# Kernel optimization log

Measured on AMD Instinct MI355X. Metric: run time of the kernel, lower is better.

Reference implementation:

```python
import jax, jax.numpy as jnp
import numpy as np
import math

B, S, D, H, DH = 2, 4096, 1024, 16, 64
CHUNK, RNDS, NBUCK, MLP = 128, 2, 64, 4096


def setup_inputs() -> dict:
    key = jax.random.key(0)
    ks = jax.random.split(key, 8)
    return {
        "inputs": jax.random.normal(ks[0], (B, S, D), jnp.float32),
        "ln1_scale": jnp.ones((D,), jnp.float32),
        "ln1_bias": jnp.zeros((D,), jnp.float32),
        "w_qk": jax.random.normal(ks[1], (D, H, DH), jnp.float32) * 0.02,
        "w_v": jax.random.normal(ks[2], (D, H, DH), jnp.float32) * 0.02,
        "w_out": jax.random.normal(ks[3], (H, DH, D), jnp.float32) * 0.02,
        "rotations": jax.random.normal(ks[4], (DH, RNDS, NBUCK // 2), jnp.float32),
        "ln2_scale": jnp.ones((D,), jnp.float32),
        "ln2_bias": jnp.zeros((D,), jnp.float32),
        "w_mlp1": jax.random.normal(ks[5], (D, MLP), jnp.float32) * 0.02,
        "b_mlp1": jnp.zeros((MLP,), jnp.float32),
        "w_mlp2": jax.random.normal(ks[6], (MLP, D), jnp.float32) * 0.02,
        "b_mlp2": jnp.zeros((D,), jnp.float32),
    }


def _layer_norm(x, scale, bias):
    mu = x.mean(-1, keepdims=True)
    var = ((x - mu) ** 2).mean(-1, keepdims=True)
    return (x - mu) / jnp.sqrt(var + 1e-6) * scale + bias


def _attend_one(q, k, v, buckets):
    # q,k,v: [S,DH]; buckets: [S] int. Sort by bucket (stable via position tiebreak),
    # chunk, attend to own chunk + 1 before + 1 after (look_both_side).
    nC = S // CHUNK
    order = jnp.argsort(buckets * S + jnp.arange(S))  # [S]
    undo = jnp.argsort(order)
    sq = q[order].reshape(nC, CHUNK, DH)
    sk = k[order].reshape(nC, CHUNK, DH)
    sv = v[order].reshape(nC, CHUNK, DH)
    st = order.reshape(nC, CHUNK)  # original token positions
    look = lambda x: jnp.concatenate([x, jnp.roll(x, 1, axis=0), jnp.roll(x, -1, axis=0)], axis=1)
    bk, bv = look(sk), look(sv)
    bt = look(st[..., None])[..., 0]
    dots = jnp.einsum('nqd,nkd->nqk', sq, bk) / math.sqrt(DH)
    # self_mask: a token attends to itself only if nothing else is available
    dots = dots - 1e5 * (st[:, :, None] == bt[:, None, :]).astype(dots.dtype)
    slog = jax.nn.logsumexp(dots, axis=-1)           # [nC,CHUNK]
    o = jnp.einsum('nqk,nkd->nqd', jax.nn.softmax(dots, axis=-1), bv)
    return o.reshape(S, DH)[undo], slog.reshape(S)[undo]


def _lsh_attention(qk, v, rotations):
    # qk,v: [B,H,S,DH]; shared-QK Reformer attention; keys are length-normalized.
    xn = qk / (jnp.linalg.norm(qk, axis=-1, keepdims=True) + 1e-6)
    rot = jnp.einsum('bhsd,drm->bhrsm', xn, rotations)          # [B,H,R,S,NBUCK/2]
    buckets = jnp.argmax(jnp.concatenate([rot, -rot], -1), -1)  # [B,H,R,S]
    rep = lambda x: jnp.broadcast_to(x[:, :, None], (B, H, RNDS, S, DH)).reshape(-1, S, DH)
    o, slog = jax.vmap(_attend_one)(rep(qk), rep(xn), rep(v), buckets.reshape(-1, S))
    o = o.reshape(B, H, RNDS, S, DH)
    slog = slog.reshape(B, H, RNDS, S)
    w = jax.nn.softmax(slog, axis=2)  # combine hash rounds by their logsumexp weight
    return (o * w[..., None]).sum(axis=2)  # [B,H,S,DH]


def reference(inputs, ln1_scale, ln1_bias, w_qk, w_v, w_out, rotations,
              ln2_scale, ln2_bias, w_mlp1, b_mlp1, w_mlp2, b_mlp2):
    x = _layer_norm(inputs, ln1_scale, ln1_bias)
    qk = jnp.einsum('bsd,dhe->bhse', x, w_qk)
    v = jnp.einsum('bsd,dhe->bhse', x, w_v)
    att = _lsh_attention(qk, v, rotations)
    x2 = inputs + jnp.einsum('bhse,hed->bsd', att, w_out)
    y = _layer_norm(x2, ln2_scale, ln2_bias)
    y = jax.nn.gelu(y @ w_mlp1 + b_mlp1) @ w_mlp2 + b_mlp2
    return x2 + y
```

## Files before the change

### kernel.cpp

```cpp
#include <hip/hip_runtime.h>
#include <hip/hip_bf16.h>


typedef short short8 __attribute__((ext_vector_type(8)));
typedef float f32x4 __attribute__((ext_vector_type(4)));
typedef unsigned short us4 __attribute__((ext_vector_type(4)));

__device__ __forceinline__ unsigned short f2bf(float f) {
  unsigned u = __builtin_bit_cast(unsigned, f);
  u += 0x7FFFu + ((u >> 16) & 1u);
  return (unsigned short)(u >> 16);
}

__device__ __forceinline__ float bf2f(unsigned short u) {
  return __builtin_bit_cast(float, ((unsigned)u) << 16);
}

__device__ __forceinline__ float gelu_f(float x) {
  float x3 = x * x * x;
  float t = tanhf(0.7978845608028654f * (x + 0.044715f * x3));
  return 0.5f * x * (1.0f + t);
}

__device__ __forceinline__ void load_lds16(const void* g, void* l) {
  __builtin_amdgcn_global_load_lds(
      (const __attribute__((address_space(1))) unsigned int*)g,
      (__attribute__((address_space(3))) unsigned int*)l, 16, 0, 0);
}

__global__ __launch_bounds__(256) void transpose_cast(
    const float* __restrict__ in, unsigned short* __restrict__ out, int R,
    int C) {
  __shared__ float tile[32][33];
  int ctiles = C >> 5;
  int bx = blockIdx.x % ctiles;
  int by = blockIdx.x / ctiles;
  int tx = threadIdx.x & 31;
  int ty = threadIdx.x >> 5;
#pragma unroll
  for (int i = 0; i < 32; i += 8)
    tile[ty + i][tx] = in[(size_t)(by * 32 + ty + i) * C + bx * 32 + tx];
  __syncthreads();
#pragma unroll
  for (int i = 0; i < 32; i += 8)
    out[(size_t)(bx * 32 + ty + i) * R + by * 32 + tx] = f2bf(tile[tx][ty + i]);
}

__global__ __launch_bounds__(256) void ln_bf16(const float* __restrict__ x,
                                               const float* __restrict__ sc,
                                               const float* __restrict__ bi,
                                               unsigned short* __restrict__ y) {
  int row = blockIdx.x, tid = threadIdx.x, lane = tid & 63, wv = tid >> 6;
  const float* xr = x + (size_t)row * 1024;
  float4 v = *(const float4*)(xr + tid * 4);
  float s1 = v.x + v.y + v.z + v.w;
  float s2 = v.x * v.x + v.y * v.y + v.z * v.z + v.w * v.w;
#pragma unroll
  for (int o = 1; o < 64; o <<= 1) {
    s1 += __shfl_xor(s1, o);
    s2 += __shfl_xor(s2, o);
  }
  __shared__ float a1[4], a2[4];
  if (lane == 0) {
    a1[wv] = s1;
    a2[wv] = s2;
  }
  __syncthreads();
  s1 = a1[0] + a1[1] + a1[2] + a1[3];
  s2 = a2[0] + a2[1] + a2[2] + a2[3];
  float mu = s1 * (1.f / 1024.f);
  float var = s2 * (1.f / 1024.f) - mu * mu;
  float rs = rsqrtf(var + 1e-6f);
  int c = tid * 4;
  us4 o4;
  o4.x = f2bf((v.x - mu) * rs * sc[c + 0] + bi[c + 0]);
  o4.y = f2bf((v.y - mu) * rs * sc[c + 1] + bi[c + 1]);
  o4.z = f2bf((v.z - mu) * rs * sc[c + 2] + bi[c + 2]);
  o4.w = f2bf((v.w - mu) * rs * sc[c + 3] + bi[c + 3]);
  *(us4*)(y + (size_t)row * 1024 + c) = o4;
}

#define GBM 128
#define GBN 128
#define GBK 32

template <int EPI>
__global__ __launch_bounds__(256) void gemm_bt(
    const unsigned short* __restrict__ A, const unsigned short* __restrict__ Bt,
    const float* __restrict__ bias, const float* __restrict__ res,
    float* __restrict__ Cf, unsigned short* __restrict__ Cb, int M, int N,
    int K) {
  __shared__ unsigned short sA[2][GBM * GBK];
  __shared__ unsigned short sB[2][GBN * GBK];
  const int nbx = N / GBN;
  const int nwg = gridDim.x;
  const int cpx = nwg >> 3;
  const int bid = blockIdx.x;
  const int swz = (bid & 7) * cpx + (bid >> 3);
  const int bx = swz % nbx;
  const int by = swz / nbx;
  const int tid = threadIdx.x;
  const int lane = tid & 63;
  const int wave = tid >> 6;
  const int wr = wave >> 1, wc = wave & 1;
  const unsigned short* Abase = A + (size_t)(by * GBM) * K;
  const unsigned short* Bbase = Bt + (size_t)(bx * GBN) * K;

  const int strow = wave * 32 + (lane >> 2);
  const int stcol = (lane & 3) * 8;
  const unsigned short* Ag = Abase + (size_t)strow * K + stcol;
  const unsigned short* Bg = Bbase + (size_t)strow * K + stcol;
  const int ldsoff = wave * 32 * GBK;
  const int ldsoff2 = ldsoff + 16 * GBK;

  f32x4 acc[4][4];
#pragma unroll
  for (int m = 0; m < 4; ++m)
#pragma unroll
    for (int n = 0; n < 4; ++n) {
      f32x4 z = {0.f, 0.f, 0.f, 0.f};
      acc[m][n] = z;
    }

  const int KT = K / GBK;
  load_lds16(Ag, &sA[0][ldsoff]);
  load_lds16(Ag + (size_t)16 * K, &sA[0][ldsoff2]);
  load_lds16(Bg, &sB[0][ldsoff]);
  load_lds16(Bg + (size_t)16 * K, &sB[0][ldsoff2]);
  __syncthreads();

  int cur = 0;
  const int arow = wr * 64 + (lane & 15);
  const int brow = wc * 64 + (lane & 15);
  const int koff = (lane >> 4) * 8;

  for (int kt = 0; kt < KT; ++kt) {
    if (kt + 1 < KT) {
      const unsigned short* An = Ag + (size_t)(kt + 1) * GBK;
      const unsigned short* Bn = Bg + (size_t)(kt + 1) * GBK;
      load_lds16(An, &sA[cur ^ 1][ldsoff]);
      load_lds16(An + (size_t)16 * K, &sA[cur ^ 1][ldsoff2]);
      load_lds16(Bn, &sB[cur ^ 1][ldsoff]);
      load_lds16(Bn + (size_t)16 * K, &sB[cur ^ 1][ldsoff2]);
    }
    short8 af[4], bfv[4];
#pragma unroll
    for (int m = 0; m < 4; ++m)
      af[m] = *(const short8*)&sA[cur][(arow + m * 16) * GBK + koff];
#pragma unroll
    for (int n = 0; n < 4; ++n)
      bfv[n] = *(const short8*)&sB[cur][(brow + n * 16) * GBK + koff];
#pragma unroll
    for (int m = 0; m < 4; ++m)
#pragma unroll
      for (int n = 0; n < 4; ++n)
        acc[m][n] = __builtin_amdgcn_mfma_f32_16x16x32_bf16(af[m], bfv[n],
                                                            acc[m][n], 0, 0, 0);
    __syncthreads();
    cur ^= 1;
  }

  const int r0 = by * GBM + wr * 64;
  const int c0 = bx * GBN + wc * 64;
#pragma unroll
  for (int m = 0; m < 4; ++m) {
#pragma unroll
    for (int n = 0; n < 4; ++n) {
#pragma unroll
      for (int i = 0; i < 4; ++i) {
        int rr = r0 + m * 16 + ((lane >> 4) << 2) + i;
        int cc = c0 + n * 16 + (lane & 15);
        float vacc = acc[m][n][i];
        if (EPI == 1) {
          float t = vacc + bias[cc];
          Cb[(size_t)rr * N + cc] = f2bf(gelu_f(t));
        } else if (EPI == 2) {
          float t = vacc + res[(size_t)rr * N + cc];
          if (bias != nullptr) t += bias[cc];
          Cf[(size_t)rr * N + cc] = t;
        } else if (EPI == 3) {
          Cf[(size_t)rr * N + cc] = vacc;
          Cb[(size_t)rr * N + cc] = f2bf(vacc);
        } else if (EPI == 4) {
          Cb[(size_t)rr * N + cc] = f2bf(vacc);
        }
      }
    }
  }
}

__global__ __launch_bounds__(256) void bucket_kernel(
    const float* __restrict__ qk, const float* __restrict__ rot,
    unsigned short* __restrict__ knb, int* __restrict__ buckets) {
  __shared__ float rotl[64 * 64];
  __shared__ float xnl[4][64];
  int tid = threadIdx.x, lane = tid & 63, wv = tid >> 6;
  for (int i = tid; i < 4096; i += 256) rotl[i] = rot[i];
  __syncthreads();
  for (int it = 0; it < 8; ++it) {
    int g = (it * 4096 + blockIdx.x) * 4 + wv;
    int bh = g >> 12;
    int s = g & 4095;
    int b = bh >> 4, h = bh & 15;
    size_t rowoff = (size_t)(b * 4096 + s) * 1024 + h * 64;
    float x = qk[rowoff + lane];
    float ss = x * x;
#pragma unroll
    for (int o = 1; o < 64; o <<= 1) ss += __shfl_xor(ss, o);
    float rn = 1.f / (sqrtf(ss) + 1e-6f);
    float xn = x * rn;
    knb[rowoff + lane] = f2bf(xn);
    xnl[wv][lane] = xn;
    __syncthreads();
    int r_ = lane >> 5, m_ = lane & 31;
    float a = 0.f;
#pragma unroll 16
    for (int d = 0; d < 64; ++d) a += xnl[wv][d] * rotl[d * 64 + r_ * 32 + m_];
    float bv;
    int bi;
    if (a >= 0.f) {
      bv = a;
      bi = m_;
    } else {
      bv = -a;
      bi = m_ + 32;
    }
#pragma unroll
    for (int o = 16; o >= 1; o >>= 1) {
      float ov = __shfl_xor(bv, o);
      int oi = __shfl_xor(bi, o);
      if (ov > bv || (ov == bv && oi < bi)) {
        bv = ov;
        bi = oi;
      }
    }
    if (m_ == 0) buckets[((size_t)bh * 2 + r_) * 4096 + s] = bi;
    __syncthreads();
  }
}

#define HSTR 65

__global__ __launch_bounds__(256) void sort_kernel(
    const int* __restrict__ buckets, int* __restrict__ order) {
  __shared__ unsigned int hist[256 * HSTR];
  __shared__ unsigned int bucketStart[64];
  const int bhr = blockIdx.x;
  const int t = threadIdx.x;
  const int* bk = buckets + (size_t)bhr * 4096;

  unsigned int* hrow = &hist[t * HSTR];
#pragma unroll
  for (int b = 0; b < 64; ++b) hrow[b] = 0u;

  int bks[16];
  {
    const int4* bp = (const int4*)(bk + t * 16);
#pragma unroll
    for (int j4 = 0; j4 < 4; ++j4) {
      int4 v = bp[j4];
      bks[j4 * 4 + 0] = v.x;
      bks[j4 * 4 + 1] = v.y;
      bks[j4 * 4 + 2] = v.z;
      bks[j4 * 4 + 3] = v.w;
    }
  }
#pragma unroll
  for (int j = 0; j < 16; ++j) hrow[bks[j]]++;
  __syncthreads();

  if (t < 64) {
    unsigned int acc = 0;
    for (int t2 = 0; t2 < 256; ++t2) {
      unsigned int c = hist[t2 * HSTR + t];
      hist[t2 * HSTR + t] = acc;
      acc += c;
    }
    bucketStart[t] = acc;
  }
  __syncthreads();
  if (t == 0) {
    unsigned int acc = 0;
    for (int b = 0; b < 64; ++b) {
      unsigned int c = bucketStart[b];
      bucketStart[b] = acc;
      acc += c;
    }
  }
  __syncthreads();

  int* op = order + (size_t)bhr * 4096;
#pragma unroll
  for (int j = 0; j < 16; ++j) {
    int b = bks[j];
    unsigned int pos = bucketStart[b] + hrow[b];
    hrow[b]++;
    op[pos] = t * 16 + j;
  }
}

#define KSTR 72
#define PSTR 136

__global__ __launch_bounds__(256, 2) void lsh_attn_mfma(
    const unsigned short* __restrict__ qb, const unsigned short* __restrict__ knb,
    const unsigned short* __restrict__ vb, const int* __restrict__ order,
    unsigned short* __restrict__ ob, float* __restrict__ slog) {
  __shared__ unsigned short Kls[128 * KSTR];
  __shared__ unsigned short Vt[64 * PSTR];
  __shared__ unsigned short Pls[4][32 * PSTR];
  __shared__ int qtokL[128];
  __shared__ int btok[128];

  const int bid = blockIdx.x;
  const int swz = (bid & 7) * 256 + (bid >> 3);
  const int c = swz & 31;
  const int bhr = swz >> 5;
  const int bh = bhr >> 1;
  const int h = bh & 15, b = bh >> 4;
  const int* ord = order + (size_t)bhr * 4096;
  const int tid = threadIdx.x, lane = tid & 63, wv = tid >> 6;
  const int l15 = lane & 15, lhi = lane >> 4;

  if (tid < 128) qtokL[tid] = ord[c * 128 + tid];
  __syncthreads();

  short8 qf[2][2];
#pragma unroll
  for (int mt = 0; mt < 2; ++mt) {
#pragma unroll
    for (int ks = 0; ks < 2; ++ks) {
      int tok = qtokL[wv * 32 + mt * 16 + l15];
      qf[mt][ks] = *(const short8*)(qb + (size_t)(b * 4096 + tok) * 1024 +
                                    h * 64 + ks * 32 + lhi * 8);
    }
  }

  float mrun[2][4], lrun[2][4];
  f32x4 oacc[2][4];
#pragma unroll
  for (int mt = 0; mt < 2; ++mt)
#pragma unroll
    for (int i = 0; i < 4; ++i) {
      mrun[mt][i] = -1e30f;
      lrun[mt][i] = 0.f;
    }
#pragma unroll
  for (int mt = 0; mt < 2; ++mt)
#pragma unroll
    for (int n = 0; n < 4; ++n) {
      f32x4 z = {0.f, 0.f, 0.f, 0.f};
      oacc[mt][n] = z;
    }

  for (int st = 0; st < 3; ++st) {
    int kc = (st == 0) ? c : (st == 1) ? ((c + 31) & 31) : ((c + 1) & 31);
    __syncthreads();
    {
      int row = tid >> 1, half = tid & 1;
      int ktok = ord[kc * 128 + row];
      if (half == 0) btok[row] = ktok;
      size_t rowoff = (size_t)(b * 4096 + ktok) * 1024 + h * 64 + half * 32;
      const short8* kp = (const short8*)(knb + rowoff);
      const short8* vp = (const short8*)(vb + rowoff);
#pragma unroll
      for (int i = 0; i < 4; ++i)
        *(short8*)&Kls[row * KSTR + half * 32 + i * 8] = kp[i];
#pragma unroll
      for (int i = 0; i < 4; ++i) {
        short8 vw = vp[i];
        int d0 = half * 32 + i * 8;
#pragma unroll
        for (int j = 0; j < 8; ++j)
          Vt[(d0 + j) * PSTR + row] = (unsigned short)vw[j];
      }
    }
    __syncthreads();

    f32x4 sacc[2][8];
#pragma unroll
    for (int mt = 0; mt < 2; ++mt)
#pragma unroll
      for (int n = 0; n < 8; ++n) {
        f32x4 z = {0.f, 0.f, 0.f, 0.f};
        sacc[mt][n] = z;
      }
#pragma unroll
    for (int ks = 0; ks < 2; ++ks) {
      short8 kf[8];
#pragma unroll
      for (int n = 0; n < 8; ++n)
        kf[n] = *(const short8*)&Kls[(n * 16 + l15) * KSTR + ks * 32 + lhi * 8];
#pragma unroll
      for (int mt = 0; mt < 2; ++mt)
#pragma unroll
        for (int n = 0; n < 8; ++n)
          sacc[mt][n] = __builtin_amdgcn_mfma_f32_16x16x32_bf16(
              qf[mt][ks], kf[n], sacc[mt][n], 0, 0, 0);
    }

    int ktA[8];
#pragma unroll
    for (int n = 0; n < 8; ++n) ktA[n] = btok[n * 16 + l15];
#pragma unroll
    for (int mt = 0; mt < 2; ++mt) {
#pragma unroll
      for (int i = 0; i < 4; ++i) {
        int qrow = wv * 32 + mt * 16 + lhi * 4 + i;
        int qt = qtokL[qrow];
        float sv[8];
        float mx = -1e30f;
#pragma unroll
        for (int n = 0; n < 8; ++n) {
          float s = sacc[mt][n][i] * 0.125f;
          if (ktA[n] == qt) s -= 1e5f;
          sv[n] = s;
          mx = fmaxf(mx, s);
        }
#pragma unroll
        for (int d = 1; d < 16; d <<= 1) mx = fmaxf(mx, __shfl_xor(mx, d));
        float mold = mrun[mt][i];
        float mnew = fmaxf(mold, mx);
        float scl = __expf(mold - mnew);
        lrun[mt][i] *= scl;
#pragma unroll
        for (int n = 0; n < 4; ++n) oacc[mt][n][i] *= scl;
        float ps = 0.f;
#pragma unroll
        for (int n = 0; n < 8; ++n) {
          float p = __expf(sv[n] - mnew);
          ps += p;
          Pls[wv][(mt * 16 + lhi * 4 + i) * PSTR + n * 16 + l15] = f2bf(p);
        }
#pragma unroll
        for (int d = 1; d < 16; d <<= 1) ps += __shfl_xor(ps, d);
        lrun[mt][i] = lrun[mt][i] + ps;
        mrun[mt][i] = mnew;
      }
    }

#pragma unroll
    for (int ks = 0; ks < 4; ++ks) {
      short8 pf[2];
#pragma unroll
      for (int mt = 0; mt < 2; ++mt)
        pf[mt] =
            *(const short8*)&Pls[wv][(mt * 16 + l15) * PSTR + ks * 32 + lhi * 8];
      short8 vfr[4];
#pragma unroll
      for (int n = 0; n < 4; ++n)
        vfr[n] = *(const short8*)&Vt[(n * 16 + l15) * PSTR + ks * 32 + lhi * 8];
#pragma unroll
      for (int mt = 0; mt < 2; ++mt)
#pragma unroll
        for (int n = 0; n < 4; ++n)
          oacc[mt][n] = __builtin_amdgcn_mfma_f32_16x16x32_bf16(
              pf[mt], vfr[n], oacc[mt][n], 0, 0, 0);
    }
  }

#pragma unroll
  for (int mt = 0; mt < 2; ++mt) {
#pragma unroll
    for (int i = 0; i < 4; ++i) {
      int qrow = wv * 32 + mt * 16 + lhi * 4 + i;
      int tok = qtokL[qrow];
      float l = lrun[mt][i];
      float invl = 1.f / l;
      if (l15 == 0) slog[(size_t)bhr * 4096 + tok] = logf(l) + mrun[mt][i];
      unsigned short* orow = ob + ((size_t)bhr * 4096 + tok) * 64;
#pragma unroll
      for (int n = 0; n < 4; ++n)
        orow[n * 16 + l15] = f2bf(oacc[mt][n][i] * invl);
    }
  }
}

__global__ __launch_bounds__(256) void combine_rounds(
    const unsigned short* __restrict__ ob, const float* __restrict__ slog,
    unsigned short* __restrict__ att) {
  int g = blockIdx.x * 4 + (threadIdx.x >> 6);
  int lane = threadIdx.x & 63;
  int h = g & 15;
  int bs = g >> 4;
  int b = bs >> 12;
  int s = bs & 4095;
  size_t base = ((size_t)(b * 16 + h) * 2) * 4096 + s;
  size_t i0 = base;
  size_t i1 = base + 4096;
  float s0 = slog[i0], s1 = slog[i1];
  float mx = fmaxf(s0, s1);
  float e0 = __expf(s0 - mx), e1 = __expf(s1 - mx);
  float w0 = e0 / (e0 + e1);
  float w1 = 1.f - w0;
  float v0 = bf2f(ob[i0 * 64 + lane]);
  float v1 = bf2f(ob[i1 * 64 + lane]);
  att[(size_t)bs * 1024 + h * 64 + lane] = f2bf(w0 * v0 + w1 * v1);
}

extern "C" void kernel_launch(void* const* d_in, const int* in_sizes, int n_in,
                              void* d_out, int out_size, void* d_ws,
                              size_t ws_size, hipStream_t stream) {
  const float* inputs = (const float*)d_in[0];
  const float* ln1s = (const float*)d_in[1];
  const float* ln1b = (const float*)d_in[2];
  const float* wqk = (const float*)d_in[3];
  const float* wv = (const float*)d_in[4];
  const float* wout = (const float*)d_in[5];
  const float* rot = (const float*)d_in[6];
  const float* ln2s = (const float*)d_in[7];
  const float* ln2b = (const float*)d_in[8];
  const float* wm1 = (const float*)d_in[9];
  const float* bm1 = (const float*)d_in[10];
  const float* wm2 = (const float*)d_in[11];
  const float* bm2 = (const float*)d_in[12];

  char* w = (char*)d_ws;
  auto alloc = [&](size_t bytes) {
    char* p = w;
    w += (bytes + 255) & ~(size_t)255;
    return p;
  };
  unsigned short* wqk_bt = (unsigned short*)alloc(1024ull * 1024 * 2);
  unsigned short* wv_bt = (unsigned short*)alloc(1024ull * 1024 * 2);
  unsigned short* wout_bt = (unsigned short*)alloc(1024ull * 1024 * 2);
  unsigned short* wm1_bt = (unsigned short*)alloc(4096ull * 1024 * 2);
  unsigned short* wm2_bt = (unsigned short*)alloc(1024ull * 4096 * 2);
  unsigned short* bufA = (unsigned short*)alloc(8192ull * 1024 * 2);
  float* qkf = (float*)alloc(8192ull * 1024 * 4);
  unsigned short* qb = (unsigned short*)alloc(8192ull * 1024 * 2);
  unsigned short* knb = (unsigned short*)alloc(8192ull * 1024 * 2);
  unsigned short* vb = (unsigned short*)alloc(8192ull * 1024 * 2);
  int* buckets = (int*)alloc(64ull * 4096 * 4);
  int* order = (int*)alloc(64ull * 4096 * 4);
  unsigned short* big =
      (unsigned short*)alloc(8192ull * 4096 * 2);
  float* slogb = (float*)alloc(64ull * 4096 * 4);
  float* x2 = qkf;
  unsigned short* obuf = big;
  unsigned short* h1 = big;

  transpose_cast<<<32 * 32, 256, 0, stream>>>(wqk, wqk_bt, 1024, 1024);
  transpose_cast<<<32 * 32, 256, 0, stream>>>(wv, wv_bt, 1024, 1024);
  transpose_cast<<<32 * 32, 256, 0, stream>>>(wout, wout_bt, 1024, 1024);
  transpose_cast<<<32 * 128, 256, 0, stream>>>(wm1, wm1_bt, 1024, 4096);
  transpose_cast<<<128 * 32, 256, 0, stream>>>(wm2, wm2_bt, 4096, 1024);

  ln_bf16<<<8192, 256, 0, stream>>>(inputs, ln1s, ln1b, bufA);

  gemm_bt<3><<<64 * 8, 256, 0, stream>>>(bufA, wqk_bt, nullptr, nullptr, qkf,
                                         qb, 8192, 1024, 1024);
  gemm_bt<4><<<64 * 8, 256, 0, stream>>>(bufA, wv_bt, nullptr, nullptr, nullptr,
                                         vb, 8192, 1024, 1024);

  bucket_kernel<<<4096, 256, 0, stream>>>(qkf, rot, knb, buckets);
  sort_kernel<<<64, 256, 0, stream>>>(buckets, order);
  lsh_attn_mfma<<<2048, 256, 0, stream>>>(qb, knb, vb, order, obuf, slogb);
  combine_rounds<<<32768, 256, 0, stream>>>(obuf, slogb, bufA);

  gemm_bt<2><<<64 * 8, 256, 0, stream>>>(bufA, wout_bt, nullptr, inputs, x2,
                                         nullptr, 8192, 1024, 1024);
  ln_bf16<<<8192, 256, 0, stream>>>(x2, ln2s, ln2b, bufA);
  gemm_bt<1><<<64 * 32, 256, 0, stream>>>(bufA, wm1_bt, bm1, nullptr, nullptr,
                                          h1, 8192, 4096, 1024);
  gemm_bt<2><<<64 * 8, 256, 0, stream>>>(h1, wm2_bt, bm2, x2, (float*)d_out,
                                         nullptr, 8192, 1024, 4096);
}
```

Baseline: 537.4 us.

## Deepen GEMM LDS pipeline to four stages with XOR swizzle and priority hints

```diff
diff --git a/kernel.cpp b/kernel.cpp
--- a/kernel.cpp
+++ b/kernel.cpp
@@ -90,8 +90,8 @@
     const float* __restrict__ bias, const float* __restrict__ res,
     float* __restrict__ Cf, unsigned short* __restrict__ Cb, int M, int N,
     int K) {
-  __shared__ unsigned short sA[2][GBM * GBK];
-  __shared__ unsigned short sB[2][GBN * GBK];
+  __shared__ unsigned short sA[4][GBM * GBK];
+  __shared__ unsigned short sB[4][GBN * GBK];
   const int nbx = N / GBN;
   const int nwg = gridDim.x;
   const int cpx = nwg >> 3;
@@ -106,10 +106,10 @@
   const unsigned short* Abase = A + (size_t)(by * GBM) * K;
   const unsigned short* Bbase = Bt + (size_t)(bx * GBN) * K;
 
-  const int strow = wave * 32 + (lane >> 2);
-  const int stcol = (lane & 3) * 8;
-  const unsigned short* Ag = Abase + (size_t)strow * K + stcol;
-  const unsigned short* Bg = Bbase + (size_t)strow * K + stcol;
+  const int srow_l = wave * 32 + (lane >> 2);
+  const int sgl = (lane & 3) ^ ((srow_l >> 1) & 3);
+  const unsigned short* Ag = Abase + (size_t)srow_l * K + sgl * 8;
+  const unsigned short* Bg = Bbase + (size_t)srow_l * K + sgl * 8;
   const int ldsoff = wave * 32 * GBK;
   const int ldsoff2 = ldsoff + 16 * GBK;
 
@@ -123,42 +123,59 @@
     }
 
   const int KT = K / GBK;
-  load_lds16(Ag, &sA[0][ldsoff]);
-  load_lds16(Ag + (size_t)16 * K, &sA[0][ldsoff2]);
-  load_lds16(Bg, &sB[0][ldsoff]);
-  load_lds16(Bg + (size_t)16 * K, &sB[0][ldsoff2]);
-  __syncthreads();
-
-  int cur = 0;
-  const int arow = wr * 64 + (lane & 15);
-  const int brow = wc * 64 + (lane & 15);
-  const int koff = (lane >> 4) * 8;
+
+#define STAGE(ktile, slot)                                             \
+  do {                                                                 \
+    const unsigned short* An_ = Ag + (size_t)(ktile)*GBK;              \
+    const unsigned short* Bn_ = Bg + (size_t)(ktile)*GBK;              \
+    load_lds16(An_, &sA[(slot)][ldsoff]);                              \
+    load_lds16(An_ + (size_t)16 * K, &sA[(slot)][ldsoff2]);            \
+    load_lds16(Bn_, &sB[(slot)][ldsoff]);                              \
+    load_lds16(Bn_ + (size_t)16 * K, &sB[(slot)][ldsoff2]);            \
+  } while (0)
+
+  STAGE(0, 0);
+  STAGE(1, 1);
+  STAGE(2, 2);
+  asm volatile("s_waitcnt vmcnt(8)" ::: "memory");
+  __builtin_amdgcn_sched_barrier(0);
+  __builtin_amdgcn_s_barrier();
+
+  const int l15 = lane & 15;
+  const int lhi = lane >> 4;
+  const int arowb = wr * 64 + l15;
+  const int browb = wc * 64 + l15;
+  const int gsw = (lhi ^ ((l15 >> 1) & 3)) * 8;
 
   for (int kt = 0; kt < KT; ++kt) {
-    if (kt + 1 < KT) {
-      const unsigned short* An = Ag + (size_t)(kt + 1) * GBK;
-      const unsigned short* Bn = Bg + (size_t)(kt + 1) * GBK;
-      load_lds16(An, &sA[cur ^ 1][ldsoff]);
-      load_lds16(An + (size_t)16 * K, &sA[cur ^ 1][ldsoff2]);
-      load_lds16(Bn, &sB[cur ^ 1][ldsoff]);
-      load_lds16(Bn + (size_t)16 * K, &sB[cur ^ 1][ldsoff2]);
-    }
+    const int slot = kt & 3;
     short8 af[4], bfv[4];
 #pragma unroll
     for (int m = 0; m < 4; ++m)
-      af[m] = *(const short8*)&sA[cur][(arow + m * 16) * GBK + koff];
+      af[m] = *(const short8*)&sA[slot][(arowb + m * 16) * GBK + gsw];
 #pragma unroll
     for (int n = 0; n < 4; ++n)
-      bfv[n] = *(const short8*)&sB[cur][(brow + n * 16) * GBK + koff];
+      bfv[n] = *(const short8*)&sB[slot][(browb + n * 16) * GBK + gsw];
+    if (kt + 3 < KT) STAGE(kt + 3, (kt + 3) & 3);
+    __builtin_amdgcn_s_setprio(1);
 #pragma unroll
     for (int m = 0; m < 4; ++m)
 #pragma unroll
       for (int n = 0; n < 4; ++n)
         acc[m][n] = __builtin_amdgcn_mfma_f32_16x16x32_bf16(af[m], bfv[n],
                                                             acc[m][n], 0, 0, 0);
-    __syncthreads();
-    cur ^= 1;
-  }
+    __builtin_amdgcn_s_setprio(0);
+    if (kt + 3 < KT) {
+      asm volatile("s_waitcnt vmcnt(8)" ::: "memory");
+    } else if (kt + 2 < KT) {
+      asm volatile("s_waitcnt vmcnt(4)" ::: "memory");
+    } else if (kt + 1 < KT) {
+      asm volatile("s_waitcnt vmcnt(0)" ::: "memory");
+    }
+    __builtin_amdgcn_sched_barrier(0);
+    __builtin_amdgcn_s_barrier();
+  }
+#undef STAGE
 
   const int r0 = by * GBM + wr * 64;
   const int c0 = bx * GBN + wc * 64;
```

New measurement: 517.3 us. -3.7%, faster.

## Fuse QK and V projections into one GEMM, add LDS swizzle and BK=64

Applied to the files above, without the earlier changes.

```diff
diff --git a/kernel.cpp b/kernel.cpp
--- a/kernel.cpp
+++ b/kernel.cpp
@@ -80,19 +80,21 @@
   *(us4*)(y + (size_t)row * 1024 + c) = o4;
 }
 
-#define GBM 128
-#define GBN 128
-#define GBK 32
-
-template <int EPI>
+
+template <int BK, int EPI>
 __global__ __launch_bounds__(256) void gemm_bt(
     const unsigned short* __restrict__ A, const unsigned short* __restrict__ Bt,
     const float* __restrict__ bias, const float* __restrict__ res,
-    float* __restrict__ Cf, unsigned short* __restrict__ Cb, int M, int N,
-    int K) {
-  __shared__ unsigned short sA[2][GBM * GBK];
-  __shared__ unsigned short sB[2][GBN * GBK];
-  const int nbx = N / GBN;
+    float* __restrict__ Cf, unsigned short* __restrict__ Cb,
+    unsigned short* __restrict__ Cb2, int M, int N, int K) {
+  constexpr int GR = BK / 8;
+  constexpr int RPS = 2048 / BK;
+  constexpr int LPM = BK / 16;
+
+  __shared__ unsigned short sA[2][128 * BK];
+  __shared__ unsigned short sB[2][128 * BK];
+
+  const int nbx = N / 128;
   const int nwg = gridDim.x;
   const int cpx = nwg >> 3;
   const int bid = blockIdx.x;
@@ -103,15 +105,14 @@
   const int lane = tid & 63;
   const int wave = tid >> 6;
   const int wr = wave >> 1, wc = wave & 1;
-  const unsigned short* Abase = A + (size_t)(by * GBM) * K;
-  const unsigned short* Bbase = Bt + (size_t)(bx * GBN) * K;
-
-  const int strow = wave * 32 + (lane >> 2);
-  const int stcol = (lane & 3) * 8;
-  const unsigned short* Ag = Abase + (size_t)strow * K + stcol;
-  const unsigned short* Bg = Bbase + (size_t)strow * K + stcol;
-  const int ldsoff = wave * 32 * GBK;
-  const int ldsoff2 = ldsoff + 16 * GBK;
+  const int l15 = lane & 15;
+  const int lhi = lane >> 4;
+
+  const int srow = tid / GR;
+  const int swzrow = (BK == 32) ? ((srow >> 1) & 3) : (srow & 7);
+  const int sgl = (tid % GR) ^ swzrow;
+  const unsigned short* Ag = A + (size_t)(by * 128 + srow) * K + sgl * 8;
+  const unsigned short* Bg = Bt + (size_t)(bx * 128 + srow) * K + sgl * 8;
 
   f32x4 acc[4][4];
 #pragma unroll
@@ -122,54 +123,62 @@
       acc[m][n] = z;
     }
 
-  const int KT = K / GBK;
-  load_lds16(Ag, &sA[0][ldsoff]);
-  load_lds16(Ag + (size_t)16 * K, &sA[0][ldsoff2]);
-  load_lds16(Bg, &sB[0][ldsoff]);
-  load_lds16(Bg + (size_t)16 * K, &sB[0][ldsoff2]);
+  const int KT = K / BK;
+
+  auto STAGE = [&](int ktile, int buf) {
+    const unsigned short* As = Ag + (size_t)ktile * BK;
+    const unsigned short* Bs = Bg + (size_t)ktile * BK;
+#pragma unroll
+    for (int i = 0; i < LPM; ++i) {
+      load_lds16(As + (size_t)i * RPS * K,
+                 (char*)&sA[buf][0] + tid * 16 + i * 4096);
+      load_lds16(Bs + (size_t)i * RPS * K,
+                 (char*)&sB[buf][0] + tid * 16 + i * 4096);
+    }
+  };
+
+  STAGE(0, 0);
   __syncthreads();
 
   int cur = 0;
-  const int arow = wr * 64 + (lane & 15);
-  const int brow = wc * 64 + (lane & 15);
-  const int koff = (lane >> 4) * 8;
+  const int arow = wr * 64 + l15;
+  const int brow = wc * 64 + l15;
 
   for (int kt = 0; kt < KT; ++kt) {
-    if (kt + 1 < KT) {
-      const unsigned short* An = Ag + (size_t)(kt + 1) * GBK;
-      const unsigned short* Bn = Bg + (size_t)(kt + 1) * GBK;
-      load_lds16(An, &sA[cur ^ 1][ldsoff]);
-      load_lds16(An + (size_t)16 * K, &sA[cur ^ 1][ldsoff2]);
-      load_lds16(Bn, &sB[cur ^ 1][ldsoff]);
-      load_lds16(Bn + (size_t)16 * K, &sB[cur ^ 1][ldsoff2]);
-    }
-    short8 af[4], bfv[4];
-#pragma unroll
-    for (int m = 0; m < 4; ++m)
-      af[m] = *(const short8*)&sA[cur][(arow + m * 16) * GBK + koff];
-#pragma unroll
-    for (int n = 0; n < 4; ++n)
-      bfv[n] = *(const short8*)&sB[cur][(brow + n * 16) * GBK + koff];
-#pragma unroll
-    for (int m = 0; m < 4; ++m)
+    if (kt + 1 < KT) STAGE(kt + 1, cur ^ 1);
+#pragma unroll
+    for (int ks = 0; ks < BK / 32; ++ks) {
+      const int physg =
+          (BK == 32) ? (lhi ^ ((l15 >> 1) & 3)) : ((ks * 4 + lhi) ^ (l15 & 7));
+      const int koff = physg * 8;
+      short8 af[4], bfv[4];
+#pragma unroll
+      for (int m = 0; m < 4; ++m)
+        af[m] = *(const short8*)&sA[cur][(arow + m * 16) * BK + koff];
 #pragma unroll
       for (int n = 0; n < 4; ++n)
-        acc[m][n] = __builtin_amdgcn_mfma_f32_16x16x32_bf16(af[m], bfv[n],
-                                                            acc[m][n], 0, 0, 0);
+        bfv[n] = *(const short8*)&sB[cur][(brow + n * 16) * BK + koff];
+#pragma unroll
+      for (int m = 0; m < 4; ++m)
+#pragma unroll
+        for (int n = 0; n < 4; ++n)
+          acc[m][n] = __builtin_amdgcn_mfma_f32_16x16x32_bf16(
+              af[m], bfv[n], acc[m][n], 0, 0, 0);
+    }
     __syncthreads();
     cur ^= 1;
   }
 
-  const int r0 = by * GBM + wr * 64;
-  const int c0 = bx * GBN + wc * 64;
+  const int r0 = by * 128 + wr * 64;
+  const int c0 = bx * 128 + wc * 64;
 #pragma unroll
   for (int m = 0; m < 4; ++m) {
 #pragma unroll
     for (int n = 0; n < 4; ++n) {
 #pragma unroll
       for (int i = 0; i < 4; ++i) {
-        int rr = r0 + m * 16 + ((lane >> 4) << 2) + i;
-        int cc = c0 + n * 16 + (lane & 15);
+        int rr = r0 + m * 16 + lhi * 4 + i;
+        int cc = c0 + n * 16 + l15;
         float vacc = acc[m][n][i];
         if (EPI == 1) {
           float t = vacc + bias[cc];
@@ -178,11 +187,13 @@
           float t = vacc + res[(size_t)rr * N + cc];
           if (bias != nullptr) t += bias[cc];
           Cf[(size_t)rr * N + cc] = t;
-        } else if (EPI == 3) {
-          Cf[(size_t)rr * N + cc] = vacc;
-          Cb[(size_t)rr * N + cc] = f2bf(vacc);
-        } else if (EPI == 4) {
-          Cb[(size_t)rr * N + cc] = f2bf(vacc);
+        } else if (EPI == 5) {
+          if (cc < 1024) {
+            Cf[(size_t)rr * 1024 + cc] = vacc;
+            Cb[(size_t)rr * 1024 + cc] = f2bf(vacc);
+          } else {
+            Cb2[(size_t)rr * 1024 + (cc - 1024)] = f2bf(vacc);
+          }
         }
       }
     }
@@ -521,8 +532,7 @@
     w += (bytes + 255) & ~(size_t)255;
     return p;
   };
-  unsigned short* wqk_bt = (unsigned short*)alloc(1024ull * 1024 * 2);
-  unsigned short* wv_bt = (unsigned short*)alloc(1024ull * 1024 * 2);
+  unsigned short* wqkv_bt = (unsigned short*)alloc(2048ull * 1024 * 2);
   unsigned short* wout_bt = (unsigned short*)alloc(1024ull * 1024 * 2);
   unsigned short* wm1_bt = (unsigned short*)alloc(4096ull * 1024 * 2);
   unsigned short* wm2_bt = (unsigned short*)alloc(1024ull * 4096 * 2);
@@ -540,29 +550,31 @@
   unsigned short* obuf = big;
   unsigned short* h1 = big;
 
-  transpose_cast<<<32 * 32, 256, 0, stream>>>(wqk, wqk_bt, 1024, 1024);
-  transpose_cast<<<32 * 32, 256, 0, stream>>>(wv, wv_bt, 1024, 1024);
+  transpose_cast<<<32 * 32, 256, 0, stream>>>(wqk, wqkv_bt, 1024, 1024);
+  transpose_cast<<<32 * 32, 256, 0, stream>>>(wv, wqkv_bt + 1024ull * 1024,
+                                              1024, 1024);
   transpose_cast<<<32 * 32, 256, 0, stream>>>(wout, wout_bt, 1024, 1024);
   transpose_cast<<<32 * 128, 256, 0, stream>>>(wm1, wm1_bt, 1024, 4096);
   transpose_cast<<<128 * 32, 256, 0, stream>>>(wm2, wm2_bt, 4096, 1024);
 
   ln_bf16<<<8192, 256, 0, stream>>>(inputs, ln1s, ln1b, bufA);
 
-  gemm_bt<3><<<64 * 8, 256, 0, stream>>>(bufA, wqk_bt, nullptr, nullptr, qkf,
-                                         qb, 8192, 1024, 1024);
-  gemm_bt<4><<<64 * 8, 256, 0, stream>>>(bufA, wv_bt, nullptr, nullptr, nullptr,
-                                         vb, 8192, 1024, 1024);
+  gemm_bt<64, 5><<<64 * 16, 256, 0, stream>>>(bufA, wqkv_bt, nullptr, nullptr,
+                                              qkf, qb, vb, 8192, 2048, 1024);
 
   bucket_kernel<<<4096, 256, 0, stream>>>(qkf, rot, knb, buckets);
   sort_kernel<<<64, 256, 0, stream>>>(buckets, order);
   lsh_attn_mfma<<<2048, 256, 0, stream>>>(qb, knb, vb, order, obuf, slogb);
   combine_rounds<<<32768, 256, 0, stream>>>(obuf, slogb, bufA);
 
-  gemm_bt<2><<<64 * 8, 256, 0, stream>>>(bufA, wout_bt, nullptr, inputs, x2,
-                                         nullptr, 8192, 1024, 1024);
+  gemm_bt<64, 2><<<64 * 8, 256, 0, stream>>>(bufA, wout_bt, nullptr, inputs,
+                                             x2, nullptr, nullptr, 8192, 1024,
+                                             1024);
   ln_bf16<<<8192, 256, 0, stream>>>(x2, ln2s, ln2b, bufA);
-  gemm_bt<1><<<64 * 32, 256, 0, stream>>>(bufA, wm1_bt, bm1, nullptr, nullptr,
-                                          h1, 8192, 4096, 1024);
-  gemm_bt<2><<<64 * 8, 256, 0, stream>>>(h1, wm2_bt, bm2, x2, (float*)d_out,
-                                         nullptr, 8192, 1024, 4096);
-}
+  gemm_bt<32, 1><<<64 * 32, 256, 0, stream>>>(bufA, wm1_bt, bm1, nullptr,
+                                              nullptr, h1, nullptr, 8192, 4096,
+                                              1024);
+  gemm_bt<64, 2><<<64 * 8, 256, 0, stream>>>(h1, wm2_bt, bm2, x2,
+                                             (float*)d_out, nullptr, nullptr,
+                                             8192, 1024, 4096);
+}
```

Result: faster. 497.8 us (-7.4%).
